# Kernel optimization log

Measured on AMD Instinct MI355X. Metric: run time of the kernel, lower is better.

## Reference

```python
import jax, jax.numpy as jnp
import numpy as np

N = 4194304          # total elements
NUM_IDS = 262144     # sorted ids drawn from [0, NUM_IDS)
M_CAP = NUM_IDS + 1  # static upper bound on number of runs (sorted input)
L_CAP = 128          # static upper bound on run length (safe for this distribution)


def setup_inputs() -> dict:
    key = jax.random.key(0)
    k1, k2 = jax.random.split(key)
    ids = jnp.sort(jax.random.randint(k1, (N,), 0, NUM_IDS, dtype=jnp.int32))
    features = jax.random.normal(k2, (N,), dtype=jnp.float32)
    return {"ids": ids, "features": features}


def _group(ids, features):
    """Run-length grouping of consecutive equal ids into a padded [M_CAP, L_CAP] layout.
    Faithful to the tf.scan original: the FINAL run is never emitted (it stays in state).
    Rows beyond the valid runs are zero-filled; their ids are -1 (the original's sentinel).
    """
    n = ids.shape[0]
    ar = jnp.arange(n, dtype=jnp.int32)
    # boundary detection -> run index per element via prefix sum
    is_start = jnp.concatenate([jnp.ones((1,), bool), ids[1:] != ids[:-1]])
    seg = jnp.cumsum(is_start.astype(jnp.int32)) - 1      # [N] run id per element
    num_runs = seg[-1] + 1
    valid_seg = seg < (num_runs - 1)                        # drop last run (scan never emits it)
    # start position of each run (segment-min of element index)
    starts = jnp.full((M_CAP,), n, dtype=jnp.int32).at[seg].min(ar)
    pos = ar - starts[seg]                                  # [N] position within run
    ok = valid_seg & (pos < L_CAP)
    seg_idx = jnp.where(ok, seg, M_CAP)                     # out-of-range -> dropped
    padded = jnp.zeros((M_CAP, L_CAP), features.dtype).at[seg_idx, pos].set(features, mode='drop')
    run_ids = jnp.full((M_CAP,), -1, dtype=ids.dtype).at[jnp.where(valid_seg, seg, M_CAP)].set(ids, mode='drop')
    return run_ids, padded


def reference(ids, features):
    return _group(ids, features)
```

## Files before the change

### kernel.cpp

```cpp
#include <hip/hip_runtime.h>

#define N_ELEM   4194304
#define NUM_IDS  262144
#define M_CAP    (NUM_IDS + 1)
#define L_CAP    128

#define NTILES   1024
#define TILE     4096
#define NTHR     256
#define EPT      16

#define WS_TICKET 0
#define WS_TOTAL  1
#define WS_TILES  4
#define META_WORDS (WS_TILES + NTILES)
#define RS_OFF    4096
#define RV_OFF    (RS_OFF + M_CAP + 3)

#define ST_SHIFT  30
#define ST_AGG    (1u << ST_SHIFT)
#define ST_PRE    (2u << ST_SHIFT)
#define VAL_MASK  ((1u << ST_SHIFT) - 1u)

#define P_TOTAL   (M_CAP * L_CAP)
#define OUT_TOTAL (M_CAP + P_TOTAL)
#define R1_F4     (NUM_IDS / 4)
#define Q0        (M_CAP + 3)
#define NF4       ((OUT_TOTAL - Q0) / 4)
#define WBLK      2048
#define WTHR      256
#define WTOT      (WBLK * WTHR)

__global__ void __launch_bounds__(NTHR)
k_scan(const int* __restrict__ ids, unsigned int* __restrict__ ws) {
    __shared__ int sm[NTHR];
    __shared__ int bc[2];

    const int t = threadIdx.x;

    if (t == 0) bc[0] = (int)atomicAdd(&ws[WS_TICKET], 1u);
    __syncthreads();
    const int vt = bc[0];
    const int base = vt * TILE + t * EPT;

    int v[EPT];
    {
        const int4* p4 = (const int4*)(ids + base);
        int4 a = p4[0], b4 = p4[1], c4 = p4[2], d4 = p4[3];
        v[0]=a.x; v[1]=a.y; v[2]=a.z; v[3]=a.w;
        v[4]=b4.x; v[5]=b4.y; v[6]=b4.z; v[7]=b4.w;
        v[8]=c4.x; v[9]=c4.y; v[10]=c4.z; v[11]=c4.w;
        v[12]=d4.x; v[13]=d4.y; v[14]=d4.z; v[15]=d4.w;
    }
    const int prev = (base == 0) ? -1 : ids[base - 1];

    unsigned flagbits = 0;
    int c = 0;
#pragma unroll
    for (int j = 0; j < EPT; ++j) {
        int f = (v[j] != ((j == 0) ? prev : v[j - 1]));
        flagbits |= ((unsigned)f << j);
        c += f;
    }

    sm[t] = c;
    __syncthreads();
    for (int off = 1; off < NTHR; off <<= 1) {
        int val = (t >= off) ? sm[t - off] : 0;
        __syncthreads();
        if (t >= off) sm[t] += val;
        __syncthreads();
    }
    const int excl = sm[t] - c;
    const int cnt  = sm[NTHR - 1];

    if (t == 0) {
        unsigned w = (vt == 0) ? (ST_PRE | (unsigned)cnt) : (ST_AGG | (unsigned)cnt);
        __hip_atomic_store(&ws[WS_TILES + vt], w, __ATOMIC_RELAXED,
                           __HIP_MEMORY_SCOPE_AGENT);
    }

    if (t < 64) {
        int prefix = 0;
        if (vt > 0) {
            int look = vt - 1;
            for (;;) {
                int idx = look - t;
                unsigned w = ST_PRE;
                if (idx >= 0)
                    w = __hip_atomic_load(&ws[WS_TILES + idx], __ATOMIC_RELAXED,
                                          __HIP_MEMORY_SCOPE_AGENT);
                unsigned st = w >> ST_SHIFT;
                unsigned long long preB = __ballot(st == 2u);
                unsigned long long invB = __ballot(st == 0u);
                if (preB) {
                    int lp = __ffsll(preB) - 1;
                    if (!(invB & ((lp > 0) ? ((1ull << lp) - 1ull) : 0ull))) {
                        int contrib = (t <= lp) ? (int)(w & VAL_MASK) : 0;
                        for (int o = 32; o; o >>= 1) contrib += __shfl_down(contrib, o);
                        prefix += __shfl(contrib, 0);
                        break;
                    }
                } else if (!invB) {
                    int contrib = (int)(w & VAL_MASK);
                    for (int o = 32; o; o >>= 1) contrib += __shfl_down(contrib, o);
                    prefix += __shfl(contrib, 0);
                    look -= 64;
                    continue;
                }
                __builtin_amdgcn_s_sleep(1);
            }
        }
        if (t == 0) {
            bc[1] = prefix;
            unsigned incl = (unsigned)(prefix + cnt);
            __hip_atomic_store(&ws[WS_TILES + vt], ST_PRE | incl,
                               __ATOMIC_RELAXED, __HIP_MEMORY_SCOPE_AGENT);
            if (vt == NTILES - 1)
                __hip_atomic_store(&ws[WS_TOTAL], incl, __ATOMIC_RELAXED,
                                   __HIP_MEMORY_SCOPE_AGENT);
        }
    }
    __syncthreads();

    {
        int* run_start = (int*)(ws + RS_OFF);
        int* run_vid   = (int*)(ws + RV_OFF);
        int rank = bc[1] + excl;
#pragma unroll
        for (int j = 0; j < EPT; ++j) {
            if (flagbits & (1u << j)) {
                run_start[rank] = base + j;
                run_vid[rank]   = v[j];
                ++rank;
            }
        }
    }
}

__global__ void __launch_bounds__(WTHR)
k_write(const unsigned int* __restrict__ ws,
        const float* __restrict__ feat,
        float* __restrict__ out) {
    const int* run_start = (const int*)(ws + RS_OFF);
    const int* run_vid   = (const int*)(ws + RV_OFF);
    const int num_valid  = (int)(ws[WS_TOTAL] & VAL_MASK) - 1;

    const int gtid = blockIdx.x * WTHR + threadIdx.x;

    if (gtid == 0) {
        out[M_CAP - 1] = -1.0f;
        int s0 = 0, L0 = 0;
        if (num_valid > 0) {
            s0 = run_start[0];
            L0 = run_start[1] - s0; if (L0 > L_CAP) L0 = L_CAP;
        }
#pragma unroll
        for (int p = 0; p < 3; ++p)
            out[M_CAP + p] = (p < L0) ? feat[s0 + p] : 0.0f;
        out[OUT_TOTAL - 1] = 0.0f;
    }

    const int total_u = R1_F4 + NF4;
    for (int u = gtid; u < total_u; u += WTOT) {
        if (u < R1_F4) {
            int4 rv = ((const int4*)run_vid)[u];
            int m = 4 * u;
            float4 r;
            r.x = (m     < num_valid) ? (float)rv.x : -1.0f;
            r.y = (m + 1 < num_valid) ? (float)rv.y : -1.0f;
            r.z = (m + 2 < num_valid) ? (float)rv.z : -1.0f;
            r.w = (m + 3 < num_valid) ? (float)rv.w : -1.0f;
            ((float4*)out)[u] = r;
        } else {
            int k = u - R1_F4;
            int p = 3 + 4 * k;
            int m0 = p >> 7, c0 = p & 127;
            int s0 = 0, L0 = 0;
            if (m0 < num_valid) {
                s0 = run_start[m0];
                L0 = run_start[m0 + 1] - s0; if (L0 > L_CAP) L0 = L_CAP;
            }
            float4 r;
            if (c0 != 127) {
                r.x = (c0     < L0) ? feat[s0 + c0]     : 0.0f;
                r.y = (c0 + 1 < L0) ? feat[s0 + c0 + 1] : 0.0f;
                r.z = (c0 + 2 < L0) ? feat[s0 + c0 + 2] : 0.0f;
                r.w = (c0 + 3 < L0) ? feat[s0 + c0 + 3] : 0.0f;
            } else {
                int m1 = m0 + 1, s1 = 0, L1 = 0;
                if (m1 < num_valid) {
                    s1 = run_start[m1];
                    L1 = run_start[m1 + 1] - s1; if (L1 > L_CAP) L1 = L_CAP;
                }
                r.x = (L0 == L_CAP) ? feat[s0 + 127] : 0.0f;
                r.y = (0 < L1) ? feat[s1]     : 0.0f;
                r.z = (1 < L1) ? feat[s1 + 1] : 0.0f;
                r.w = (2 < L1) ? feat[s1 + 2] : 0.0f;
            }
            *(float4*)(out + Q0 + 4 * (size_t)k) = r;
        }
    }
}

extern "C" void kernel_launch(void* const* d_in, const int* in_sizes, int n_in,
                              void* d_out, int out_size, void* d_ws, size_t ws_size,
                              hipStream_t stream) {
    const int* ids    = (const int*)d_in[0];
    const float* feat = (const float*)d_in[1];
    float* out        = (float*)d_out;
    unsigned int* ws  = (unsigned int*)d_ws;

    hipMemsetAsync(ws, 0, META_WORDS * sizeof(unsigned int), stream);

    k_scan<<<NTILES, NTHR, 0, stream>>>(ids, ws);
    k_write<<<WBLK, WTHR, 0, stream>>>(ws, feat, out);
}
```

Measured before the change: 216.7 us.

## Split write kernel into per-block row tiles with shared run_start cache

The write kernel is reorganised so that each of 2048 blocks owns 128 padded output rows and first stages the 130 run_start entries it needs into shared memory, instead of every thread gathering run_start from global memory in a grid-stride loop. Separate blocks handle the run_ids section and the tail row. The scan kernel now stores run ids already converted to float so the writer only copies them. This removes repeated global loads of run boundaries and simplifies indexing, but it adds a block barrier and extra boundary handling for the shifted output layout.

```diff
diff --git a/kernel.cpp b/kernel.cpp
--- a/kernel.cpp
+++ b/kernel.cpp
@@ -24,12 +24,9 @@
 
 #define P_TOTAL   (M_CAP * L_CAP)
 #define OUT_TOTAL (M_CAP + P_TOTAL)
-#define R1_F4     (NUM_IDS / 4)
-#define Q0        (M_CAP + 3)
-#define NF4       ((OUT_TOTAL - Q0) / 4)
-#define WBLK      2048
+#define PAD_BLK   2048
+#define RID_BLK   16
 #define WTHR      256
-#define WTOT      (WBLK * WTHR)
 
 __global__ void __launch_bounds__(NTHR)
 k_scan(const int* __restrict__ ids, unsigned int* __restrict__ ws) {
@@ -124,14 +121,14 @@
     __syncthreads();
 
     {
-        int* run_start = (int*)(ws + RS_OFF);
-        int* run_vid   = (int*)(ws + RV_OFF);
+        int*   run_start = (int*)(ws + RS_OFF);
+        float* run_vid_f = (float*)(ws + RV_OFF);
         int rank = bc[1] + excl;
 #pragma unroll
         for (int j = 0; j < EPT; ++j) {
             if (flagbits & (1u << j)) {
                 run_start[rank] = base + j;
-                run_vid[rank]   = v[j];
+                run_vid_f[rank] = (float)v[j];
                 ++rank;
             }
         }
@@ -142,45 +139,31 @@
 k_write(const unsigned int* __restrict__ ws,
         const float* __restrict__ feat,
         float* __restrict__ out) {
-    const int* run_start = (const int*)(ws + RS_OFF);
-    const int* run_vid   = (const int*)(ws + RV_OFF);
-    const int num_valid  = (int)(ws[WS_TOTAL] & VAL_MASK) - 1;
-
-    const int gtid = blockIdx.x * WTHR + threadIdx.x;
-
-    if (gtid == 0) {
-        out[M_CAP - 1] = -1.0f;
-        int s0 = 0, L0 = 0;
-        if (num_valid > 0) {
-            s0 = run_start[0];
-            L0 = run_start[1] - s0; if (L0 > L_CAP) L0 = L_CAP;
-        }
-#pragma unroll
-        for (int p = 0; p < 3; ++p)
-            out[M_CAP + p] = (p < L0) ? feat[s0 + p] : 0.0f;
-        out[OUT_TOTAL - 1] = 0.0f;
-    }
-
-    const int total_u = R1_F4 + NF4;
-    for (int u = gtid; u < total_u; u += WTOT) {
-        if (u < R1_F4) {
-            int4 rv = ((const int4*)run_vid)[u];
-            int m = 4 * u;
-            float4 r;
-            r.x = (m     < num_valid) ? (float)rv.x : -1.0f;
-            r.y = (m + 1 < num_valid) ? (float)rv.y : -1.0f;
-            r.z = (m + 2 < num_valid) ? (float)rv.z : -1.0f;
-            r.w = (m + 3 < num_valid) ? (float)rv.w : -1.0f;
-            ((float4*)out)[u] = r;
-        } else {
-            int k = u - R1_F4;
-            int p = 3 + 4 * k;
-            int m0 = p >> 7, c0 = p & 127;
-            int s0 = 0, L0 = 0;
-            if (m0 < num_valid) {
-                s0 = run_start[m0];
-                L0 = run_start[m0 + 1] - s0; if (L0 > L_CAP) L0 = L_CAP;
-            }
+    const int*   run_start = (const int*)(ws + RS_OFF);
+    const float* run_vid_f = (const float*)(ws + RV_OFF);
+    const int num_valid    = (int)(ws[WS_TOTAL] & VAL_MASK) - 1;
+
+    const int b = blockIdx.x;
+    const int t = threadIdx.x;
+
+    if (b < PAD_BLK) {
+        __shared__ int sm[130];
+        const int rb = b * 128;
+        if (t < 130) sm[t] = run_start[rb + t];
+        __syncthreads();
+
+        float* obase = out + M_CAP + (size_t)rb * L_CAP;
+#pragma unroll 4
+        for (int i = 0; i < 16; ++i) {
+            const int j  = t + i * WTHR;
+            const int pl = 3 + 4 * j;
+            const int m  = pl >> 7;
+            const int c0 = pl & 127;
+
+            int s0 = sm[m];
+            int L0 = sm[m + 1] - s0; if (L0 > L_CAP) L0 = L_CAP;
+            if (rb + m >= num_valid) L0 = 0;
+
             float4 r;
             if (c0 != 127) {
                 r.x = (c0     < L0) ? feat[s0 + c0]     : 0.0f;
@@ -188,18 +171,48 @@
                 r.z = (c0 + 2 < L0) ? feat[s0 + c0 + 2] : 0.0f;
                 r.w = (c0 + 3 < L0) ? feat[s0 + c0 + 3] : 0.0f;
             } else {
-                int m1 = m0 + 1, s1 = 0, L1 = 0;
-                if (m1 < num_valid) {
-                    s1 = run_start[m1];
-                    L1 = run_start[m1 + 1] - s1; if (L1 > L_CAP) L1 = L_CAP;
-                }
+                int s1 = sm[m + 1];
+                int L1 = sm[m + 2] - s1; if (L1 > L_CAP) L1 = L_CAP;
+                if (rb + m + 1 >= num_valid) L1 = 0;
                 r.x = (L0 == L_CAP) ? feat[s0 + 127] : 0.0f;
                 r.y = (0 < L1) ? feat[s1]     : 0.0f;
                 r.z = (1 < L1) ? feat[s1 + 1] : 0.0f;
                 r.w = (2 < L1) ? feat[s1 + 2] : 0.0f;
             }
-            *(float4*)(out + Q0 + 4 * (size_t)k) = r;
-        }
+            *(float4*)(obase + pl) = r;
+        }
+    } else if (b < PAD_BLK + RID_BLK) {
+        const int ub = (b - PAD_BLK) * 4096;
+#pragma unroll 4
+        for (int i = 0; i < 16; ++i) {
+            const int u = ub + t + i * WTHR;
+            float4 rv = ((const float4*)run_vid_f)[u];
+            const int m = 4 * u;
+            float4 r;
+            r.x = (m     < num_valid) ? rv.x : -1.0f;
+            r.y = (m + 1 < num_valid) ? rv.y : -1.0f;
+            r.z = (m + 2 < num_valid) ? rv.z : -1.0f;
+            r.w = (m + 3 < num_valid) ? rv.w : -1.0f;
+            ((float4*)out)[u] = r;
+        }
+    } else {
+        if (t == 0) {
+            out[M_CAP - 1] = -1.0f;
+            int s0 = 0, L0 = 0;
+            if (num_valid > 0) {
+                s0 = run_start[0];
+                L0 = run_start[1] - s0; if (L0 > L_CAP) L0 = L_CAP;
+            }
+#pragma unroll
+            for (int p = 0; p < 3; ++p)
+                out[M_CAP + p] = (p < L0) ? feat[s0 + p] : 0.0f;
+        }
+        const size_t base = (size_t)M_CAP + (size_t)262144 * L_CAP;
+        if (t < 31) {
+            float4 z = {0.0f, 0.0f, 0.0f, 0.0f};
+            *(float4*)(out + base + 3 + 4 * t) = z;
+        }
+        if (t == 31) out[base + 127] = 0.0f;
     }
 }
 
@@ -214,5 +227,5 @@
     hipMemsetAsync(ws, 0, META_WORDS * sizeof(unsigned int), stream);
 
     k_scan<<<NTILES, NTHR, 0, stream>>>(ids, ws);
-    k_write<<<WBLK, WTHR, 0, stream>>>(ws, feat, out);
+    k_write<<<PAD_BLK + RID_BLK + 1, WTHR, 0, stream>>>(ws, feat, out);
 }
```

New measurement: 197.5 us. 8.9% less time.

## Fuse run scan and padded write into one kernel using LDS run tables

Applied to the files above, without the earlier changes.

Merges the scan kernel and the write kernel into one. Each tile keeps its run starts and ids in LDS, looks ahead into the next tile to find where its last run ends, and then writes its own rows of the padded output once its decoupled-lookback prefix is known. This removes the global run_start/run_vid round trip and one kernel launch. In exchange, write bandwidth now rests on only 1024 blocks, the final tile serially fills the tail padding, and the larger LDS footprint may lower occupancy.

```diff
diff --git a/kernel.cpp b/kernel.cpp
--- a/kernel.cpp
+++ b/kernel.cpp
@@ -11,11 +11,8 @@
 #define EPT      16
 
 #define WS_TICKET 0
-#define WS_TOTAL  1
 #define WS_TILES  4
 #define META_WORDS (WS_TILES + NTILES)
-#define RS_OFF    4096
-#define RV_OFF    (RS_OFF + M_CAP + 3)
 
 #define ST_SHIFT  30
 #define ST_AGG    (1u << ST_SHIFT)
@@ -23,25 +20,26 @@
 #define VAL_MASK  ((1u << ST_SHIFT) - 1u)
 
 #define P_TOTAL   (M_CAP * L_CAP)
-#define OUT_TOTAL (M_CAP + P_TOTAL)
-#define R1_F4     (NUM_IDS / 4)
-#define Q0        (M_CAP + 3)
-#define NF4       ((OUT_TOTAL - Q0) / 4)
-#define WBLK      2048
-#define WTHR      256
-#define WTOT      (WBLK * WTHR)
+#define OUT_TOTAL ((size_t)M_CAP + P_TOTAL)
 
 __global__ void __launch_bounds__(NTHR)
-k_scan(const int* __restrict__ ids, unsigned int* __restrict__ ws) {
-    __shared__ int sm[NTHR];
-    __shared__ int bc[2];
+k_fused(const int* __restrict__ ids,
+        const float* __restrict__ feat,
+        float* __restrict__ out,
+        unsigned int* __restrict__ ws) {
+    __shared__ int   sm[NTHR];
+    __shared__ int   bc[2];
+    __shared__ int   lds_start[TILE + 1];
+    __shared__ float lds_vid[TILE];
 
     const int t = threadIdx.x;
 
     if (t == 0) bc[0] = (int)atomicAdd(&ws[WS_TICKET], 1u);
     __syncthreads();
     const int vt = bc[0];
-    const int base = vt * TILE + t * EPT;
+    const int tile_base = vt * TILE;
+    const int tile_end  = tile_base + TILE;
+    const int base      = tile_base + t * EPT;
 
     int v[EPT];
     {
@@ -78,6 +76,42 @@
         unsigned w = (vt == 0) ? (ST_PRE | (unsigned)cnt) : (ST_AGG | (unsigned)cnt);
         __hip_atomic_store(&ws[WS_TILES + vt], w, __ATOMIC_RELAXED,
                            __HIP_MEMORY_SCOPE_AGENT);
+    }
+
+    {
+        int r = excl;
+#pragma unroll
+        for (int j = 0; j < EPT; ++j) {
+            if (flagbits & (1u << j)) {
+                lds_start[r] = base + j;
+                lds_vid[r]   = (float)v[j];
+                ++r;
+            }
+        }
+    }
+    __syncthreads();
+
+    if (t >= 64 && t < 128) {
+        if (cnt > 0) {
+            int e = tile_end;
+            if (vt != NTILES - 1) {
+                int s_last = lds_start[cnt - 1];
+                if (tile_end - s_last < L_CAP) {
+                    int vid = (int)lds_vid[cnt - 1];
+                    int l = t - 64;
+                    int m0 = (ids[tile_end + l]      != vid);
+                    int m1 = (ids[tile_end + l + 64] != vid);
+                    unsigned long long b0 = __ballot(m0);
+                    unsigned long long b1 = __ballot(m1);
+                    int ext;
+                    if (b0)      ext = __ffsll(b0) - 1;
+                    else if (b1) ext = 64 + __ffsll(b1) - 1;
+                    else         ext = 128;
+                    e = tile_end + ext;
+                }
+            }
+            if (t == 64) lds_start[cnt] = e;
+        }
     }
 
     if (t < 64) {
@@ -113,74 +147,41 @@
         }
         if (t == 0) {
             bc[1] = prefix;
-            unsigned incl = (unsigned)(prefix + cnt);
-            __hip_atomic_store(&ws[WS_TILES + vt], ST_PRE | incl,
+            __hip_atomic_store(&ws[WS_TILES + vt],
+                               ST_PRE | (unsigned)(prefix + cnt),
                                __ATOMIC_RELAXED, __HIP_MEMORY_SCOPE_AGENT);
-            if (vt == NTILES - 1)
-                __hip_atomic_store(&ws[WS_TOTAL], incl, __ATOMIC_RELAXED,
-                                   __HIP_MEMORY_SCOPE_AGENT);
-        }
-    }
-    __syncthreads();
-
-    {
-        int* run_start = (int*)(ws + RS_OFF);
-        int* run_vid   = (int*)(ws + RV_OFF);
-        int rank = bc[1] + excl;
-#pragma unroll
-        for (int j = 0; j < EPT; ++j) {
-            if (flagbits & (1u << j)) {
-                run_start[rank] = base + j;
-                run_vid[rank]   = v[j];
-                ++rank;
-            }
-        }
-    }
-}
-
-__global__ void __launch_bounds__(WTHR)
-k_write(const unsigned int* __restrict__ ws,
-        const float* __restrict__ feat,
-        float* __restrict__ out) {
-    const int* run_start = (const int*)(ws + RS_OFF);
-    const int* run_vid   = (const int*)(ws + RV_OFF);
-    const int num_valid  = (int)(ws[WS_TOTAL] & VAL_MASK) - 1;
-
-    const int gtid = blockIdx.x * WTHR + threadIdx.x;
-
-    if (gtid == 0) {
-        out[M_CAP - 1] = -1.0f;
-        int s0 = 0, L0 = 0;
-        if (num_valid > 0) {
-            s0 = run_start[0];
-            L0 = run_start[1] - s0; if (L0 > L_CAP) L0 = L_CAP;
-        }
-#pragma unroll
-        for (int p = 0; p < 3; ++p)
-            out[M_CAP + p] = (p < L0) ? feat[s0 + p] : 0.0f;
-        out[OUT_TOTAL - 1] = 0.0f;
-    }
-
-    const int total_u = R1_F4 + NF4;
-    for (int u = gtid; u < total_u; u += WTOT) {
-        if (u < R1_F4) {
-            int4 rv = ((const int4*)run_vid)[u];
-            int m = 4 * u;
-            float4 r;
-            r.x = (m     < num_valid) ? (float)rv.x : -1.0f;
-            r.y = (m + 1 < num_valid) ? (float)rv.y : -1.0f;
-            r.z = (m + 2 < num_valid) ? (float)rv.z : -1.0f;
-            r.w = (m + 3 < num_valid) ? (float)rv.w : -1.0f;
-            ((float4*)out)[u] = r;
-        } else {
-            int k = u - R1_F4;
-            int p = 3 + 4 * k;
-            int m0 = p >> 7, c0 = p & 127;
-            int s0 = 0, L0 = 0;
-            if (m0 < num_valid) {
-                s0 = run_start[m0];
-                L0 = run_start[m0 + 1] - s0; if (L0 > L_CAP) L0 = L_CAP;
-            }
+        }
+    }
+    __syncthreads();
+
+    const int prefix = bc[1];
+    int cnt_emit = (vt == NTILES - 1) ? cnt - 1 : cnt;
+    if (cnt_emit < 0) cnt_emit = 0;
+
+    for (int r = t; r < cnt_emit; r += NTHR)
+        out[prefix + r] = lds_vid[r];
+
+    const size_t q_lo = (size_t)M_CAP + (size_t)prefix * L_CAP;
+    if (cnt_emit > 0) {
+        if (t < 3) {
+            int s0 = lds_start[0];
+            int L0 = lds_start[1] - s0; if (L0 > L_CAP) L0 = L_CAP;
+            out[q_lo + t] = (t < L0) ? feat[s0 + t] : 0.0f;
+        }
+        if (t == 3) {
+            int sL = lds_start[cnt_emit - 1];
+            int LL = lds_start[cnt_emit] - sL; if (LL > L_CAP) LL = L_CAP;
+            out[q_lo + (size_t)cnt_emit * L_CAP - 1] =
+                (LL == L_CAP) ? feat[sL + 127] : 0.0f;
+        }
+        float* qa = out + q_lo + 3;
+        const int nf4 = cnt_emit * 32 - 1;
+        for (int u = t; u < nf4; u += NTHR) {
+            const int pl = 3 + 4 * u;
+            const int lm = pl >> 7;
+            const int c0 = pl & 127;
+            int s0 = lds_start[lm];
+            int L0 = lds_start[lm + 1] - s0; if (L0 > L_CAP) L0 = L_CAP;
             float4 r;
             if (c0 != 127) {
                 r.x = (c0     < L0) ? feat[s0 + c0]     : 0.0f;
@@ -188,18 +189,24 @@
                 r.z = (c0 + 2 < L0) ? feat[s0 + c0 + 2] : 0.0f;
                 r.w = (c0 + 3 < L0) ? feat[s0 + c0 + 3] : 0.0f;
             } else {
-                int m1 = m0 + 1, s1 = 0, L1 = 0;
-                if (m1 < num_valid) {
-                    s1 = run_start[m1];
-                    L1 = run_start[m1 + 1] - s1; if (L1 > L_CAP) L1 = L_CAP;
-                }
+                int s1 = lds_start[lm + 1];
+                int L1 = lds_start[lm + 2] - s1; if (L1 > L_CAP) L1 = L_CAP;
                 r.x = (L0 == L_CAP) ? feat[s0 + 127] : 0.0f;
                 r.y = (0 < L1) ? feat[s1]     : 0.0f;
                 r.z = (1 < L1) ? feat[s1 + 1] : 0.0f;
                 r.w = (2 < L1) ? feat[s1 + 2] : 0.0f;
             }
-            *(float4*)(out + Q0 + 4 * (size_t)k) = r;
-        }
+            *(float4*)(qa + 4 * (size_t)u) = r;
+        }
+    }
+
+    if (vt == NTILES - 1) {
+        const int num_valid = prefix + cnt_emit;
+        for (int i = num_valid + t; i < M_CAP; i += NTHR)
+            out[i] = -1.0f;
+        const size_t p0 = (size_t)M_CAP + (size_t)num_valid * L_CAP;
+        for (size_t p = p0 + t; p < OUT_TOTAL; p += NTHR)
+            out[p] = 0.0f;
     }
 }
 
@@ -213,6 +220,5 @@
 
     hipMemsetAsync(ws, 0, META_WORDS * sizeof(unsigned int), stream);
 
-    k_scan<<<NTILES, NTHR, 0, stream>>>(ids, ws);
-    k_write<<<WBLK, WTHR, 0, stream>>>(ws, feat, out);
+    k_fused<<<NTILES, NTHR, 0, stream>>>(ids, feat, out, ws);
 }
```

Result: faster. 210.4 us (-2.9%).
